# Performance work log

Hardware: AMD Instinct MI355X
Metric: run time of the kernel (lower is better)

Reference implementation:

```python
import jax, jax.numpy as jnp
import numpy as np

B, C, T, K = 16, 512, 2048, 64

def setup_inputs() -> dict:
    key = jax.random.key(0)
    k1, k2, k3 = jax.random.split(key, 3)
    v = jax.random.normal(k1, (B, C, T), dtype=jnp.float32)
    # 1x1 Conv1d weights == linear maps over channel dim
    Wk = jax.random.normal(k2, (K, C), dtype=jnp.float32) * 0.02
    bk = jnp.zeros((K,), dtype=jnp.float32)
    Wq = jax.random.normal(k3, (K, C), dtype=jnp.float32) * 0.02
    bq = jnp.zeros((K,), dtype=jnp.float32)
    gamma = jnp.ones((), dtype=jnp.float32)
    return {"v": v, "Wk": Wk, "bk": bk, "Wq": Wq, "bq": bq, "gamma": gamma}

def reference(v, Wk, bk, Wq, bq, gamma):
    # k, q: (B, K, T) via 1x1 conv = channel-wise linear
    k = jnp.einsum('kc,bct->bkt', Wk, v) + bk[None, :, None]
    q = jnp.einsum('kc,bct->bkt', Wq, v) + bq[None, :, None]
    # original: e1[b,d,i,j]=q[b,d,j], e2[b,d,i,j]=k[b,d,i]; sum over d
    # -> s[b,i,j] = sum_d k[b,d,i] * q[b,d,j]  (avoid materializing B,K,T,T)
    s = jnp.einsum('bdi,bdj->bij', k, q)  # (B, T, T)
    a = jax.nn.softmax(s, axis=1)          # softmax over dim=1 (the i axis)
    att = jnp.einsum('bct,btj->bcj', v, a)  # bmm(v, a)
    return v + gamma * att
```

## Files before the change

### kernel.cpp

```cpp
#include <hip/hip_runtime.h>

#define Bc 16
#define Cc 512
#define Tc 2048
#define QT 128
#define KT 64
#define PST 72
#define LTS 66

typedef __attribute__((ext_vector_type(8))) short short8;
typedef __attribute__((ext_vector_type(4))) float f32x4;
typedef unsigned short u16;

static __device__ __forceinline__ u16 f2bf(float x) {
  unsigned u = __float_as_uint(x);
  u += 0x7FFF + ((u >> 16) & 1);
  return (u16)(u >> 16);
}

static __device__ __forceinline__ unsigned cvt_pk_bf16(float lo, float hi) {
  unsigned r;
  asm("v_cvt_pk_bf16_f32 %0, %1, %2" : "=v"(r) : "v"(lo), "v"(hi));
  return r;
}

static __device__ __forceinline__ void block_sync_lds() {
  __builtin_amdgcn_sched_barrier(0);
  asm volatile("s_waitcnt lgkmcnt(0)" ::: "memory");
  __builtin_amdgcn_s_barrier();
  __builtin_amdgcn_sched_barrier(0);
}

__global__ __launch_bounds__(256) void prep_kernel(
    const float* __restrict__ Wk, const float* __restrict__ Wq,
    const float* __restrict__ bk, const float* __restrict__ bq,
    u16* __restrict__ Wbf, float* __restrict__ bkq)
{
  int idx  = blockIdx.x * 256 + threadIdx.x;
  int base = idx * 4;
  if (base < 128 * Cc) {
    int ch = base >> 9;
    int c  = base & (Cc - 1);
    const float* src = (ch < 64) ? (Wk + (size_t)ch * Cc + c)
                                 : (Wq + (size_t)(ch - 64) * Cc + c);
    f32x4 w = *reinterpret_cast<const f32x4*>(src);
    uint2 o;
    o.x = (unsigned)f2bf(w[0]) | ((unsigned)f2bf(w[1]) << 16);
    o.y = (unsigned)f2bf(w[2]) | ((unsigned)f2bf(w[3]) << 16);
    *reinterpret_cast<uint2*>(Wbf + base) = o;
  }
  if (idx < 128) bkq[idx] = (idx < 64) ? bk[idx] : bq[idx - 64];
}

__global__ __launch_bounds__(256) void kqv_kernel(
    const float* __restrict__ v, const u16* __restrict__ Wbf,
    const float* __restrict__ bkq, u16* __restrict__ kq, u16* __restrict__ vbf)
{
  __shared__ u16 LDSt[2][64][LTS];
  const int b   = blockIdx.y;
  const int t0  = blockIdx.x * 64;
  const int tid = threadIdx.x;
  const int lane = tid & 63;
  const int w    = tid >> 6;
  const int l15  = lane & 15;
  const int lg   = lane >> 4;

  f32x4 acc[8];
  #pragma unroll
  for (int mt = 0; mt < 8; ++mt) acc[mt] = f32x4{0.f, 0.f, 0.f, 0.f};

  const float* vb = v + (size_t)b * Cc * Tc + t0;
  float x[16];
  #pragma unroll
  for (int r = 0; r < 16; ++r) x[r] = vb[(size_t)(w * 16 + r) * Tc + lane];

  int buf = 0;
  for (int c0 = 0; c0 < Cc; c0 += 64, buf ^= 1) {
    #pragma unroll
    for (int r = 0; r < 16; ++r) {
      u16 hb = f2bf(x[r]);
      LDSt[buf][lane][w * 16 + r] = hb;
      vbf[((size_t)b * Cc + c0 + w * 16 + r) * Tc + t0 + lane] = hb;
    }
    block_sync_lds();
    if (c0 + 64 < Cc) {
      #pragma unroll
      for (int r = 0; r < 16; ++r)
        x[r] = vb[(size_t)(c0 + 64 + w * 16 + r) * Tc + lane];
    }
    #pragma unroll
    for (int ks = 0; ks < 2; ++ks) {
      short8 bfrag = *reinterpret_cast<const short8*>(&LDSt[buf][w * 16 + l15][ks * 32 + lg * 8]);
      #pragma unroll
      for (int mt = 0; mt < 8; ++mt) {
        short8 afrag = *reinterpret_cast<const short8*>(
            Wbf + (size_t)(mt * 16 + l15) * Cc + c0 + ks * 32 + lg * 8);
        acc[mt] = __builtin_amdgcn_mfma_f32_16x16x32_bf16(afrag, bfrag, acc[mt], 0, 0, 0);
      }
    }
  }
  const int t = t0 + w * 16 + l15;
  u16* op = kq + ((size_t)b * Tc + t) * 128;
  #pragma unroll
  for (int mt = 0; mt < 8; ++mt) {
    int chb = mt * 16 + lg * 4;
    uint2 o;
    o.x = cvt_pk_bf16(acc[mt][0] + bkq[chb + 0], acc[mt][1] + bkq[chb + 1]);
    o.y = cvt_pk_bf16(acc[mt][2] + bkq[chb + 2], acc[mt][3] + bkq[chb + 3]);
    *reinterpret_cast<uint2*>(op + chb) = o;
  }
}

__global__ __launch_bounds__(512, 2) void attn_kernel(
    const float* __restrict__ v, const u16* __restrict__ vbf,
    const u16* __restrict__ kq, const float* __restrict__ gamma_p,
    float* __restrict__ out)
{
  __shared__ u16 P[2][QT * PST];
  __shared__ float lsum_lds[QT];

  const int L   = blockIdx.x;
  const int lin = (L & 7) * 32 + (L >> 3);
  const int b   = lin >> 4;
  const int j0  = (lin & 15) * QT;
  const int tid = threadIdx.x;
  const int lane = tid & 63;
  const int wid  = tid >> 6;
  const int l15  = lane & 15;
  const int lg   = lane >> 4;
  const int c0   = wid * 64;

  short8 qf0, qf1;
  {
    const u16* qp = kq + (size_t)(b * Tc + j0 + wid * 16 + l15) * 128 + 64 + lg * 8;
    qf0 = *reinterpret_cast<const short8*>(qp);
    qf1 = *reinterpret_cast<const short8*>(qp + 32);
  }

  f32x4 O[4][8];
  #pragma unroll
  for (int a = 0; a < 4; ++a)
    #pragma unroll
    for (int bb = 0; bb < 8; ++bb) O[a][bb] = f32x4{0.f, 0.f, 0.f, 0.f};

  float lsum = 0.f;

  const u16* kbase = kq + (size_t)b * Tc * 128 + lg * 8;
  const u16* vbase = vbf + ((size_t)b * Cc + c0) * Tc;

  short8 kf[4][2];
  short8 vf0[4];

  #pragma unroll
  for (int it = 0; it < 4; ++it) {
    const u16* kp = kbase + (size_t)(it * 16 + l15) * 128;
    kf[it][0] = *reinterpret_cast<const short8*>(kp);
    kf[it][1] = *reinterpret_cast<const short8*>(kp + 32);
  }
  #pragma unroll
  for (int ct = 0; ct < 4; ++ct)
    vf0[ct] = *reinterpret_cast<const short8*>(
        vbase + (size_t)(ct * 16 + l15) * Tc + lg * 8);
  {
    f32x4 sacc[4];
    #pragma unroll
    for (int it = 0; it < 4; ++it) {
      f32x4 s = f32x4{0.f, 0.f, 0.f, 0.f};
      s = __builtin_amdgcn_mfma_f32_16x16x32_bf16(kf[it][0], qf0, s, 0, 0, 0);
      s = __builtin_amdgcn_mfma_f32_16x16x32_bf16(kf[it][1], qf1, s, 0, 0, 0);
      sacc[it] = s;
    }
    u16* prow = &P[0][(wid * 16 + l15) * PST];
    #pragma unroll
    for (int it = 0; it < 4; ++it) {
      float p0 = __expf(sacc[it][0]);
      float p1 = __expf(sacc[it][1]);
      float p2 = __expf(sacc[it][2]);
      float p3 = __expf(sacc[it][3]);
      lsum += (p0 + p1) + (p2 + p3);
      uint2 wv;
      wv.x = cvt_pk_bf16(p0, p1);
      wv.y = cvt_pk_bf16(p2, p3);
      *reinterpret_cast<uint2*>(prow + it * 16 + lg * 4) = wv;
    }
  }
  #pragma unroll
  for (int it = 0; it < 4; ++it) {
    const u16* kp = kbase + (size_t)(KT + it * 16 + l15) * 128;
    kf[it][0] = *reinterpret_cast<const short8*>(kp);
    kf[it][1] = *reinterpret_cast<const short8*>(kp + 32);
  }
  block_sync_lds();

  int pb = 0;
  for (int i0 = 0; i0 < Tc; i0 += KT, pb ^= 1) {
    const bool last = (i0 + KT >= Tc);

    short8 vf1[4];
    #pragma unroll
    for (int ct = 0; ct < 4; ++ct)
      vf1[ct] = *reinterpret_cast<const short8*>(
          vbase + (size_t)(ct * 16 + l15) * Tc + i0 + 32 + lg * 8);

    if (!last) {
      f32x4 sacc[4];
      #pragma unroll
      for (int it = 0; it < 4; ++it) {
        f32x4 s = f32x4{0.f, 0.f, 0.f, 0.f};
        s = __builtin_amdgcn_mfma_f32_16x16x32_bf16(kf[it][0], qf0, s, 0, 0, 0);
        s = __builtin_amdgcn_mfma_f32_16x16x32_bf16(kf[it][1], qf1, s, 0, 0, 0);
        sacc[it] = s;
      }
      u16* prow = &P[pb ^ 1][(wid * 16 + l15) * PST];
      #pragma unroll
      for (int it = 0; it < 4; ++it) {
        float p0 = __expf(sacc[it][0]);
        float p1 = __expf(sacc[it][1]);
        float p2 = __expf(sacc[it][2]);
        float p3 = __expf(sacc[it][3]);
        lsum += (p0 + p1) + (p2 + p3);
        uint2 wv;
        wv.x = cvt_pk_bf16(p0, p1);
        wv.y = cvt_pk_bf16(p2, p3);
        *reinterpret_cast<uint2*>(prow + it * 16 + lg * 4) = wv;
      }
    }

    __builtin_amdgcn_s_setprio(1);
    {
      short8 pf[8];
      #pragma unroll
      for (int jj = 0; jj < 8; ++jj)
        pf[jj] = *reinterpret_cast<const short8*>(
            &P[pb][(jj * 16 + l15) * PST + lg * 8]);
      #pragma unroll
      for (int ct = 0; ct < 4; ++ct)
        #pragma unroll
        for (int jj = 0; jj < 8; ++jj)
          O[ct][jj] = __builtin_amdgcn_mfma_f32_16x16x32_bf16(vf0[ct], pf[jj], O[ct][jj], 0, 0, 0);
    }
    {
      short8 pf[8];
      #pragma unroll
      for (int jj = 0; jj < 8; ++jj)
        pf[jj] = *reinterpret_cast<const short8*>(
            &P[pb][(jj * 16 + l15) * PST + 32 + lg * 8]);
      #pragma unroll
      for (int ct = 0; ct < 4; ++ct)
        #pragma unroll
        for (int jj = 0; jj < 8; ++jj)
          O[ct][jj] = __builtin_amdgcn_mfma_f32_16x16x32_bf16(vf1[ct], pf[jj], O[ct][jj], 0, 0, 0);
    }
    __builtin_amdgcn_s_setprio(0);

    if (!last) {
      if (i0 + 2 * KT < Tc) {
        #pragma unroll
        for (int it = 0; it < 4; ++it) {
          const u16* kp = kbase + (size_t)(i0 + 2 * KT + it * 16 + l15) * 128;
          kf[it][0] = *reinterpret_cast<const short8*>(kp);
          kf[it][1] = *reinterpret_cast<const short8*>(kp + 32);
        }
      }
      #pragma unroll
      for (int ct = 0; ct < 4; ++ct)
        vf0[ct] = *reinterpret_cast<const short8*>(
            vbase + (size_t)(ct * 16 + l15) * Tc + (i0 + KT) + lg * 8);
      block_sync_lds();
    }
  }

  lsum += __shfl_xor(lsum, 16);
  lsum += __shfl_xor(lsum, 32);
  if (lane < 16) lsum_lds[wid * 16 + lane] = lsum;
  __syncthreads();
  const float gamma = *gamma_p;
  #pragma unroll
  for (int jj = 0; jj < 8; ++jj) {
    float linv = gamma / lsum_lds[jj * 16 + l15];
    int j = j0 + jj * 16 + l15;
    #pragma unroll
    for (int ct = 0; ct < 4; ++ct) {
      #pragma unroll
      for (int r = 0; r < 4; ++r) {
        int c = c0 + ct * 16 + lg * 4 + r;
        size_t idx = (size_t)(b * Cc + c) * Tc + j;
        out[idx] = v[idx] + linv * O[ct][jj][r];
      }
    }
  }
}

extern "C" void kernel_launch(void* const* d_in, const int* in_sizes, int n_in,
                              void* d_out, int out_size, void* d_ws, size_t ws_size,
                              hipStream_t stream) {
  const float* v  = (const float*)d_in[0];
  const float* Wk = (const float*)d_in[1];
  const float* bk = (const float*)d_in[2];
  const float* Wq = (const float*)d_in[3];
  const float* bq = (const float*)d_in[4];
  const float* gm = (const float*)d_in[5];
  float* out = (float*)d_out;

  char* ws = (char*)d_ws;
  u16*   kqb = (u16*)ws;
  u16*   vbf = (u16*)(ws + 8388608);
  u16*   Wbf = (u16*)(ws + 8388608 + 33554432);
  float* bkq = (float*)(ws + 8388608 + 33554432 + 131072);

  prep_kernel<<<dim3(64), dim3(256), 0, stream>>>(Wk, Wq, bk, bq, Wbf, bkq);
  kqv_kernel<<<dim3(Tc / 64, Bc), dim3(256), 0, stream>>>(v, Wbf, bkq, kqb, vbf);
  attn_kernel<<<dim3((Tc / QT) * Bc), dim3(512), 0, stream>>>(v, vbf, kqb, gm, out);
}
```

Baseline: 192.6 us.

## Switch PV matmul to 32x32x16 MFMA with XOR-swizzled P and LDS-staged epilogue

Replaces the 16x16x32 MFMAs in the attention-times-V accumulation with 32x32x16 bf16 MFMAs, so each wave issues fewer, larger matrix instructions with more operand reuse. The padded P layout becomes an unpadded 64-wide layout with an XOR chunk swizzle to avoid LDS bank conflicts. The epilogue now stages accumulators through per-wave LDS so that v reads and out writes are vectorised float4 and coalesced, instead of scattered scalar accesses. Costs are extra LDS (about 36KB for epilogue staging), which may hurt occupancy at 2 blocks per CU, and the setprio hints are dropped.

```diff
diff --git a/kernel.cpp b/kernel.cpp
--- a/kernel.cpp
+++ b/kernel.cpp
@@ -5,11 +5,11 @@
 #define Tc 2048
 #define QT 128
 #define KT 64
-#define PST 72
 #define LTS 66
 
-typedef __attribute__((ext_vector_type(8))) short short8;
-typedef __attribute__((ext_vector_type(4))) float f32x4;
+typedef __attribute__((ext_vector_type(8)))  short short8;
+typedef __attribute__((ext_vector_type(4)))  float f32x4;
+typedef __attribute__((ext_vector_type(16))) float f32x16;
 typedef unsigned short u16;
 
 static __device__ __forceinline__ u16 f2bf(float x) {
@@ -116,8 +116,10 @@
     const u16* __restrict__ kq, const float* __restrict__ gamma_p,
     float* __restrict__ out)
 {
-  __shared__ u16 P[2][QT * PST];
+  __shared__ u16 P[2][128 * 64];
+  __shared__ __align__(16) float ep_lds[8][32 * 36];
   __shared__ float lsum_lds[QT];
+  __shared__ __align__(16) float linv_lds[QT];
 
   const int L   = blockIdx.x;
   const int lin = (L & 7) * 32 + (L >> 3);
@@ -128,6 +130,8 @@
   const int wid  = tid >> 6;
   const int l15  = lane & 15;
   const int lg   = lane >> 4;
+  const int l31  = lane & 31;
+  const int kh   = lane >> 5;
   const int c0   = wid * 64;
 
   short8 qf0, qf1;
@@ -137,11 +141,13 @@
     qf1 = *reinterpret_cast<const short8*>(qp + 32);
   }
 
-  f32x4 O[4][8];
-  #pragma unroll
-  for (int a = 0; a < 4; ++a)
-    #pragma unroll
-    for (int bb = 0; bb < 8; ++bb) O[a][bb] = f32x4{0.f, 0.f, 0.f, 0.f};
+  f32x16 O32[2][4];
+  #pragma unroll
+  for (int a = 0; a < 2; ++a)
+    #pragma unroll
+    for (int bb = 0; bb < 4; ++bb)
+      #pragma unroll
+      for (int e = 0; e < 16; ++e) O32[a][bb][e] = 0.f;
 
   float lsum = 0.f;
 
@@ -149,7 +155,8 @@
   const u16* vbase = vbf + ((size_t)b * Cc + c0) * Tc;
 
   short8 kf[4][2];
-  short8 vf0[4];
+  short8 vf0[2][2];
+  const int vrow = (size_t)0 + l31;
 
   #pragma unroll
   for (int it = 0; it < 4; ++it) {
@@ -158,9 +165,11 @@
     kf[it][1] = *reinterpret_cast<const short8*>(kp + 32);
   }
   #pragma unroll
-  for (int ct = 0; ct < 4; ++ct)
-    vf0[ct] = *reinterpret_cast<const short8*>(
-        vbase + (size_t)(ct * 16 + l15) * Tc + lg * 8);
+  for (int ct = 0; ct < 2; ++ct)
+    #pragma unroll
+    for (int kk = 0; kk < 2; ++kk)
+      vf0[ct][kk] = *reinterpret_cast<const short8*>(
+          vbase + (size_t)(ct * 32 + vrow) * Tc + kk * 16 + kh * 8);
   {
     f32x4 sacc[4];
     #pragma unroll
@@ -170,7 +179,7 @@
       s = __builtin_amdgcn_mfma_f32_16x16x32_bf16(kf[it][1], qf1, s, 0, 0, 0);
       sacc[it] = s;
     }
-    u16* prow = &P[0][(wid * 16 + l15) * PST];
+    u16* prow = &P[0][(wid * 16 + l15) * 64];
     #pragma unroll
     for (int it = 0; it < 4; ++it) {
       float p0 = __expf(sacc[it][0]);
@@ -181,7 +190,8 @@
       uint2 wv;
       wv.x = cvt_pk_bf16(p0, p1);
       wv.y = cvt_pk_bf16(p2, p3);
-      *reinterpret_cast<uint2*>(prow + it * 16 + lg * 4) = wv;
+      int chk = ((it * 2 + (lg >> 1)) ^ (l15 & 7)) * 8 + (lg & 1) * 4;
+      *reinterpret_cast<uint2*>(prow + chk) = wv;
     }
   }
   #pragma unroll
@@ -196,11 +206,13 @@
   for (int i0 = 0; i0 < Tc; i0 += KT, pb ^= 1) {
     const bool last = (i0 + KT >= Tc);
 
-    short8 vf1[4];
-    #pragma unroll
-    for (int ct = 0; ct < 4; ++ct)
-      vf1[ct] = *reinterpret_cast<const short8*>(
-          vbase + (size_t)(ct * 16 + l15) * Tc + i0 + 32 + lg * 8);
+    short8 vf1[2][2];
+    #pragma unroll
+    for (int ct = 0; ct < 2; ++ct)
+      #pragma unroll
+      for (int kk = 0; kk < 2; ++kk)
+        vf1[ct][kk] = *reinterpret_cast<const short8*>(
+            vbase + (size_t)(ct * 32 + vrow) * Tc + i0 + 32 + kk * 16 + kh * 8);
 
     if (!last) {
       f32x4 sacc[4];
@@ -211,7 +223,7 @@
         s = __builtin_amdgcn_mfma_f32_16x16x32_bf16(kf[it][1], qf1, s, 0, 0, 0);
         sacc[it] = s;
       }
-      u16* prow = &P[pb ^ 1][(wid * 16 + l15) * PST];
+      u16* prow = &P[pb ^ 1][(wid * 16 + l15) * 64];
       #pragma unroll
       for (int it = 0; it < 4; ++it) {
         float p0 = __expf(sacc[it][0]);
@@ -222,36 +234,28 @@
         uint2 wv;
         wv.x = cvt_pk_bf16(p0, p1);
         wv.y = cvt_pk_bf16(p2, p3);
-        *reinterpret_cast<uint2*>(prow + it * 16 + lg * 4) = wv;
-      }
-    }
-
-    __builtin_amdgcn_s_setprio(1);
-    {
-      short8 pf[8];
-      #pragma unroll
-      for (int jj = 0; jj < 8; ++jj)
-        pf[jj] = *reinterpret_cast<const short8*>(
-            &P[pb][(jj * 16 + l15) * PST + lg * 8]);
-      #pragma unroll
-      for (int ct = 0; ct < 4; ++ct)
-        #pragma unroll
-        for (int jj = 0; jj < 8; ++jj)
-          O[ct][jj] = __builtin_amdgcn_mfma_f32_16x16x32_bf16(vf0[ct], pf[jj], O[ct][jj], 0, 0, 0);
-    }
-    {
-      short8 pf[8];
-      #pragma unroll
-      for (int jj = 0; jj < 8; ++jj)
-        pf[jj] = *reinterpret_cast<const short8*>(
-            &P[pb][(jj * 16 + l15) * PST + 32 + lg * 8]);
-      #pragma unroll
-      for (int ct = 0; ct < 4; ++ct)
-        #pragma unroll
-        for (int jj = 0; jj < 8; ++jj)
-          O[ct][jj] = __builtin_amdgcn_mfma_f32_16x16x32_bf16(vf1[ct], pf[jj], O[ct][jj], 0, 0, 0);
-    }
-    __builtin_amdgcn_s_setprio(0);
+        int chk = ((it * 2 + (lg >> 1)) ^ (l15 & 7)) * 8 + (lg & 1) * 4;
+        *reinterpret_cast<uint2*>(prow + chk) = wv;
+      }
+    }
+
+    #pragma unroll
+    for (int ks = 0; ks < 4; ++ks) {
+      short8 pf[4];
+      #pragma unroll
+      for (int jt = 0; jt < 4; ++jt) {
+        int row = jt * 32 + l31;
+        int chk = ((ks * 2 + kh) ^ (row & 7)) * 8;
+        pf[jt] = *reinterpret_cast<const short8*>(&P[pb][row * 64 + chk]);
+      }
+      const short8* vsel0 = (ks < 2) ? &vf0[0][ks] : &vf1[0][ks - 2];
+      const short8* vsel1 = (ks < 2) ? &vf0[1][ks] : &vf1[1][ks - 2];
+      #pragma unroll
+      for (int jt = 0; jt < 4; ++jt) {
+        O32[0][jt] = __builtin_amdgcn_mfma_f32_32x32x16_bf16(*vsel0, pf[jt], O32[0][jt], 0, 0, 0);
+        O32[1][jt] = __builtin_amdgcn_mfma_f32_32x32x16_bf16(*vsel1, pf[jt], O32[1][jt], 0, 0, 0);
+      }
+    }
 
     if (!last) {
       if (i0 + 2 * KT < Tc) {
@@ -263,9 +267,11 @@
         }
       }
       #pragma unroll
-      for (int ct = 0; ct < 4; ++ct)
-        vf0[ct] = *reinterpret_cast<const short8*>(
-            vbase + (size_t)(ct * 16 + l15) * Tc + (i0 + KT) + lg * 8);
+      for (int ct = 0; ct < 2; ++ct)
+        #pragma unroll
+        for (int kk = 0; kk < 2; ++kk)
+          vf0[ct][kk] = *reinterpret_cast<const short8*>(
+              vbase + (size_t)(ct * 32 + vrow) * Tc + (i0 + KT) + kk * 16 + kh * 8);
       block_sync_lds();
     }
   }
@@ -275,18 +281,42 @@
   if (lane < 16) lsum_lds[wid * 16 + lane] = lsum;
   __syncthreads();
   const float gamma = *gamma_p;
-  #pragma unroll
-  for (int jj = 0; jj < 8; ++jj) {
-    float linv = gamma / lsum_lds[jj * 16 + l15];
-    int j = j0 + jj * 16 + l15;
-    #pragma unroll
-    for (int ct = 0; ct < 4; ++ct) {
-      #pragma unroll
-      for (int r = 0; r < 4; ++r) {
-        int c = c0 + ct * 16 + lg * 4 + r;
-        size_t idx = (size_t)(b * Cc + c) * Tc + j;
-        out[idx] = v[idx] + linv * O[ct][jj][r];
-      }
+  if (tid < QT) linv_lds[tid] = gamma / lsum_lds[tid];
+  __syncthreads();
+
+  float* ep = ep_lds[wid];
+  const int rd_row = lane >> 3;
+  const int rd_ch  = lane & 7;
+  #pragma unroll
+  for (int ct = 0; ct < 2; ++ct) {
+    #pragma unroll
+    for (int jt = 0; jt < 4; ++jt) {
+      #pragma unroll
+      for (int reg = 0; reg < 16; ++reg) {
+        int cl = (reg & 3) + 8 * (reg >> 2) + 4 * kh;
+        ep[cl * 36 + l31] = O32[ct][jt][reg];
+      }
+      asm volatile("s_waitcnt lgkmcnt(0)" ::: "memory");
+      __builtin_amdgcn_sched_barrier(0);
+      #pragma unroll
+      for (int h = 0; h < 4; ++h) {
+        const int row = rd_row + 8 * h;
+        f32x4 o4 = *reinterpret_cast<const f32x4*>(&ep[row * 36 + rd_ch * 4]);
+        const int jg = jt * 32 + rd_ch * 4;
+        f32x4 li = *reinterpret_cast<const f32x4*>(&linv_lds[jg]);
+        const int c_glob = c0 + ct * 32 + row;
+        const float* vr = v + ((size_t)(b * Cc + c_glob)) * Tc + j0 + jg;
+        float* orow = out + ((size_t)(b * Cc + c_glob)) * Tc + j0 + jg;
+        f32x4 v4 = *reinterpret_cast<const f32x4*>(vr);
+        f32x4 o;
+        o[0] = v4[0] + li[0] * o4[0];
+        o[1] = v4[1] + li[1] * o4[1];
+        o[2] = v4[2] + li[2] * o4[2];
+        o[3] = v4[3] + li[3] * o4[3];
+        *reinterpret_cast<f32x4*>(orow) = o;
+      }
+      asm volatile("s_waitcnt lgkmcnt(0)" ::: "memory");
+      __builtin_amdgcn_sched_barrier(0);
     }
   }
 }
```

New measurement: 191.0 us. Within noise of the previous version (-0.8%).
